# Kernel optimization log

Measured on AMD Instinct MI355X. Metric: run time of the kernel, lower is better.

The kernel has to match this reference:

```python
import jax, jax.numpy as jnp
import numpy as np

D_MODEL = 1024
NUM_HEADS = 16
D_K = D_MODEL // NUM_HEADS
CLAMP = 1e9
EPS = 1e-12


def setup_inputs() -> dict:
    key = jax.random.key(0)
    ks = jax.random.split(key, 11)
    B, S, D = 4, 2048, D_MODEL
    std = 1.0 / np.sqrt(D)
    inp = {
        'Q': jax.random.normal(ks[0], (B, S, D), jnp.float32),
        'K': jax.random.normal(ks[1], (B, S, D), jnp.float32),
        'V': jax.random.normal(ks[2], (B, S, D), jnp.float32),
        'Wq': jax.random.normal(ks[3], (D, D), jnp.float32) * std,
        'bq': jnp.zeros((D,), jnp.float32),
        'Wk': jax.random.normal(ks[4], (D, D), jnp.float32) * std,
        'bk': jnp.zeros((D,), jnp.float32),
        'Wv': jax.random.normal(ks[5], (D, D), jnp.float32) * std,
        'bv': jnp.zeros((D,), jnp.float32),
        'Wo': jax.random.normal(ks[6], (D, D), jnp.float32) * std,
        'bo': jnp.zeros((D,), jnp.float32),
    }
    return inp


def _split_heads(x):
    b, s, _ = x.shape
    return x.reshape(b, s, NUM_HEADS, D_K).transpose(0, 2, 1, 3)  # [b,h,s,dk]


def reference(Q, K, V, Wq, bq, Wk, bk, Wv, bv, Wo, bo):
    Qh = _split_heads(Q @ Wq.T + bq)
    Kh = _split_heads(K @ Wk.T + bk)
    Vh = _split_heads(V @ Wv.T + bv)
    scale = jnp.sqrt(jnp.asarray(D_K, Qh.dtype))
    scores = jnp.einsum('bhqd,bhkd->bhqk', Qh, Kh) / scale
    scores = scores - jnp.max(scores, axis=-1, keepdims=True)
    scores = jnp.clip(scores, -CLAMP, CLAMP)
    attn = jax.nn.softmax(scores, axis=-1)
    attn = jnp.clip(attn, EPS, None)
    attn = attn / jnp.sum(attn, axis=-1, keepdims=True)
    ctx = jnp.einsum('bhqk,bhkd->bhqd', attn, Vh)
    b, h, s, dk = ctx.shape
    ctx = ctx.transpose(0, 2, 1, 3).reshape(b, s, D_MODEL)
    return ctx @ Wo.T + bo
```

## Files before the change

kernel.cpp:

```cpp
#include <hip/hip_runtime.h>
#include <hip/hip_bf16.h>


typedef float  f32x4  __attribute__((ext_vector_type(4)));
typedef __bf16 bf16x8 __attribute__((ext_vector_type(8)));
typedef short  s16x8  __attribute__((ext_vector_type(8)));
typedef int    i32x4  __attribute__((ext_vector_type(4)));

#define MFMA16(a,b,c) __builtin_amdgcn_mfma_f32_16x16x32_bf16((a),(b),(c),0,0,0)

__device__ __forceinline__ unsigned short f2bf(float f) {
    union { float f; unsigned u; } v; v.f = f;
    unsigned r = v.u + 0x7fffu + ((v.u >> 16) & 1u);
    return (unsigned short)(r >> 16);
}

__device__ __forceinline__ s16x8 cvt8(const float* __restrict__ p) {
    f32x4 x = *(const f32x4*)p;
    f32x4 y = *(const f32x4*)(p + 4);
    s16x8 r;
    r[0] = (short)f2bf(x[0]); r[1] = (short)f2bf(x[1]);
    r[2] = (short)f2bf(x[2]); r[3] = (short)f2bf(x[3]);
    r[4] = (short)f2bf(y[0]); r[5] = (short)f2bf(y[1]);
    r[6] = (short)f2bf(y[2]); r[7] = (short)f2bf(y[3]);
    return r;
}

__device__ __forceinline__ void gl_lds16(const void* g, void* l) {
    __builtin_amdgcn_global_load_lds(
        (const __attribute__((address_space(1))) unsigned int*)g,
        (__attribute__((address_space(3))) unsigned int*)l, 16, 0, 0);
}

__device__ __forceinline__ int cvtpk_bf16(float lo, float hi) {
    int r;
    asm("v_cvt_pk_bf16_f32 %0, %1, %2" : "=v"(r) : "v"(lo), "v"(hi));
    return r;
}
__device__ __forceinline__ void plswap32(int& a, int& b) {
    asm("v_permlane32_swap_b32 %0, %1" : "+v"(a), "+v"(b));
}
__device__ __forceinline__ void plswap16(int& a, int& b) {
    asm("v_permlane16_swap_b32 %0, %1" : "+v"(a), "+v"(b));
}

__global__ __launch_bounds__(256) void cvt_kernel(
    const float* __restrict__ src, unsigned short* __restrict__ dst, int n8)
{
    int i = blockIdx.x * 256 + threadIdx.x;
    if (i < n8) *(s16x8*)(dst + (size_t)i * 8) = cvt8(src + (size_t)i * 8);
}

template <int MODE>
__global__ __launch_bounds__(256) void gemm_bf16(
    const unsigned short* __restrict__ A,
    const unsigned short* __restrict__ W,
    const float* __restrict__ bias,
    void* __restrict__ Cv)
{
    constexpr int K = 1024;
    __shared__ unsigned short Ash[128 * 32];
    __shared__ unsigned short Bsh[128 * 32];

    const int t    = threadIdx.x;
    const int w    = t >> 6;
    const int lane = t & 63;
    const int wm   = w >> 1, wn = w & 1;
    const int lr   = lane & 15, quad = lane >> 4;

    const int m0 = blockIdx.y * 128;
    const int n0 = blockIdx.x * 128;

    const int srow = t >> 2;
    const int skp  = (t & 3) * 8;

    const unsigned short* Ap0 = A + (size_t)(m0 + srow) * K + skp;
    const unsigned short* Ap1 = Ap0 + (size_t)64 * K;
    const unsigned short* Wp0 = W + (size_t)(n0 + srow) * K + skp;
    const unsigned short* Wp1 = Wp0 + (size_t)64 * K;
    unsigned short* lA0 = &Ash[w * 512];
    unsigned short* lA1 = &Ash[2048 + w * 512];
    unsigned short* lB0 = &Bsh[w * 512];
    unsigned short* lB1 = &Bsh[2048 + w * 512];

    f32x4 acc[4][4] = {};

    for (int k0 = 0; k0 < K; k0 += 32) {
        __syncthreads();
        gl_lds16(Ap0 + k0, lA0);
        gl_lds16(Ap1 + k0, lA1);
        gl_lds16(Wp0 + k0, lB0);
        gl_lds16(Wp1 + k0, lB1);
        __syncthreads();

        bf16x8 af[4], bw[4];
#pragma unroll
        for (int i = 0; i < 4; i++)
            af[i] = *(const bf16x8*)&Ash[(wm * 64 + i * 16 + lr) * 32 + quad * 8];
#pragma unroll
        for (int j = 0; j < 4; j++)
            bw[j] = *(const bf16x8*)&Bsh[(wn * 64 + j * 16 + lr) * 32 + quad * 8];

#pragma unroll
        for (int i = 0; i < 4; i++)
#pragma unroll
            for (int j = 0; j < 4; j++)
                acc[i][j] = MFMA16(af[i], bw[j], acc[i][j]);
    }

#pragma unroll
    for (int i = 0; i < 4; i++) {
#pragma unroll
        for (int j = 0; j < 4; j++) {
            const int n = n0 + wn * 64 + j * 16 + lr;
#pragma unroll
            for (int r = 0; r < 4; r++) {
                const int m = m0 + wm * 64 + i * 16 + quad * 4 + r;
                float val = acc[i][j][r] + ((MODE == 2) ? bias[m] : bias[n]);
                if (MODE == 0) {
                    const int b = m >> 11, s = m & 2047, h = n >> 6, d = n & 63;
                    ((unsigned short*)Cv)[(((size_t)(b * 16 + h) * 2048 + s) << 6) + d] = f2bf(val);
                } else if (MODE == 1) {
                    ((float*)Cv)[(size_t)m * 1024 + n] = val;
                } else {
                    const int h = m >> 6, d = m & 63, b = n >> 11, s = n & 2047;
                    ((unsigned short*)Cv)[((size_t)(b * 16 + h) * 64 + d) * 2048 + s] = f2bf(val);
                }
            }
        }
    }
}

__global__ __launch_bounds__(256) void attn_kernel(
    const unsigned short* __restrict__ Qh,
    const unsigned short* __restrict__ Kh,
    const unsigned short* __restrict__ Vt,
    unsigned short* __restrict__ ctx)
{
    constexpr int KS = 72;
    __shared__ unsigned short Ksh[64 * KS];
    __shared__ unsigned short Vts[64 * KS];

    const int t    = threadIdx.x;
    const int w    = t >> 6;
    const int lane = t & 63;
    const int lr   = lane & 15, quad = lane >> 4;

    const int bh = blockIdx.y, qblk = blockIdx.x;
    const size_t base = (size_t)bh * 2048 * 64;
    const unsigned short* Qp = Qh + base;
    const unsigned short* Kg = Kh + base + (size_t)lane * 64 + w * 16;
    const unsigned short* Vg = Vt + base + (size_t)lane * 2048 + w * 16;

    const int q0 = qblk * 64 + w * 16;
    bf16x8 aq0 = *(const bf16x8*)(Qp + (size_t)(q0 + lr) * 64 + quad * 8);
    bf16x8 aq1 = *(const bf16x8*)(Qp + (size_t)(q0 + lr) * 64 + 32 + quad * 8);

    f32x4 Of[4] = {};
    float lsum = 0.f;

    s16x8 kv0 = *(const s16x8*)(Kg);
    s16x8 kv1 = *(const s16x8*)(Kg + 8);
    s16x8 vv0 = *(const s16x8*)(Vg);
    s16x8 vv1 = *(const s16x8*)(Vg + 8);

    for (int kb = 0; kb < 2048; kb += 64) {
        __syncthreads();
        *(s16x8*)&Ksh[lane * KS + w * 16]     = kv0;
        *(s16x8*)&Ksh[lane * KS + w * 16 + 8] = kv1;
        *(s16x8*)&Vts[lane * KS + w * 16]     = vv0;
        *(s16x8*)&Vts[lane * KS + w * 16 + 8] = vv1;

        const int kn = (kb + 64) & 2047;
        kv0 = *(const s16x8*)(Kg + (size_t)kn * 64);
        kv1 = *(const s16x8*)(Kg + (size_t)kn * 64 + 8);
        vv0 = *(const s16x8*)(Vg + kn);
        vv1 = *(const s16x8*)(Vg + kn + 8);

        __syncthreads();

        f32x4 pe[4];
#pragma unroll
        for (int nt = 0; nt < 4; nt++) {
            const unsigned short* kr = &Ksh[(16 * nt + lr) * KS + quad * 8];
            f32x4 c = {};
            c = MFMA16(*(const bf16x8*)kr, aq0, c);
            c = MFMA16(*(const bf16x8*)(kr + 32), aq1, c);
            f32x4 p;
#pragma unroll
            for (int r = 0; r < 4; r++) p[r] = __expf(c[r] * 0.125f);
            lsum += (p[0] + p[1]) + (p[2] + p[3]);
            pe[nt] = p;
        }

        int a0 = cvtpk_bf16(pe[0][0], pe[0][1]);
        int a1 = cvtpk_bf16(pe[0][2], pe[0][3]);
        int b0 = cvtpk_bf16(pe[1][0], pe[1][1]);
        int b1 = cvtpk_bf16(pe[1][2], pe[1][3]);
        plswap32(a0, b0); plswap32(a1, b1);
        plswap16(a0, b0); plswap16(a1, b1);
        i32x4 f0; f0[0] = a0; f0[1] = a1; f0[2] = b0; f0[3] = b1;

        int c0 = cvtpk_bf16(pe[2][0], pe[2][1]);
        int c1 = cvtpk_bf16(pe[2][2], pe[2][3]);
        int d0 = cvtpk_bf16(pe[3][0], pe[3][1]);
        int d1 = cvtpk_bf16(pe[3][2], pe[3][3]);
        plswap32(c0, d0); plswap32(c1, d1);
        plswap16(c0, d0); plswap16(c1, d1);
        i32x4 f1; f1[0] = c0; f1[1] = c1; f1[2] = d0; f1[3] = d1;

        bf16x8 pf0 = __builtin_bit_cast(bf16x8, f0);
        bf16x8 pf1 = __builtin_bit_cast(bf16x8, f1);

#pragma unroll
        for (int dt = 0; dt < 4; dt++) {
            const unsigned short* vr = &Vts[(dt * 16 + lr) * KS + quad * 8];
            Of[dt] = MFMA16(pf0, *(const bf16x8*)vr, Of[dt]);
            Of[dt] = MFMA16(pf1, *(const bf16x8*)(vr + 32), Of[dt]);
        }
    }

    lsum += __shfl_xor(lsum, 16);
    lsum += __shfl_xor(lsum, 32);

    const int b = bh >> 4, h = bh & 15;
#pragma unroll
    for (int r = 0; r < 4; r++) {
        const float inv = 1.0f / __shfl(lsum, quad * 4 + r, 64);
        const int q = q0 + quad * 4 + r;
        unsigned short* cp = ctx + ((size_t)b * 2048 + q) * 1024 + h * 64;
#pragma unroll
        for (int dt = 0; dt < 4; dt++)
            cp[dt * 16 + lr] = f2bf(Of[dt][r] * inv);
    }
}

extern "C" void kernel_launch(void* const* d_in, const int* in_sizes, int n_in,
                              void* d_out, int out_size, void* d_ws, size_t ws_size,
                              hipStream_t stream) {
    const float* Q  = (const float*)d_in[0];
    const float* K  = (const float*)d_in[1];
    const float* V  = (const float*)d_in[2];
    const float* Wq = (const float*)d_in[3];
    const float* bq = (const float*)d_in[4];
    const float* Wk = (const float*)d_in[5];
    const float* bk = (const float*)d_in[6];
    const float* Wv = (const float*)d_in[7];
    const float* bv = (const float*)d_in[8];
    const float* Wo = (const float*)d_in[9];
    const float* bo = (const float*)d_in[10];

    const size_t EB = (size_t)8192 * 1024;
    const size_t EW = (size_t)1024 * 1024;
    unsigned short* Xb  = (unsigned short*)d_ws;
    unsigned short* Wqb = Xb  + EB;
    unsigned short* Wkb = Wqb + EW;
    unsigned short* Wvb = Wkb + EW;
    unsigned short* Wob = Wvb + EW;
    unsigned short* Qh  = Wob + EW;
    unsigned short* Kh  = Qh  + EB;
    unsigned short* Vtw = Kh  + EB;
    unsigned short* Ctx = Xb;

    const int n8b = (int)(EB / 8);
    const int n8w = (int)(EW / 8);

    cvt_kernel<<<n8w / 256, 256, 0, stream>>>(Wq, Wqb, n8w);
    cvt_kernel<<<n8w / 256, 256, 0, stream>>>(Wk, Wkb, n8w);
    cvt_kernel<<<n8w / 256, 256, 0, stream>>>(Wv, Wvb, n8w);
    cvt_kernel<<<n8w / 256, 256, 0, stream>>>(Wo, Wob, n8w);

    dim3 tb(256), gP(8, 64), gT(64, 8);

    cvt_kernel<<<n8b / 256, 256, 0, stream>>>(Q, Xb, n8b);
    gemm_bf16<0><<<gP, tb, 0, stream>>>(Xb, Wqb, bq, Qh);

    cvt_kernel<<<n8b / 256, 256, 0, stream>>>(K, Xb, n8b);
    gemm_bf16<0><<<gP, tb, 0, stream>>>(Xb, Wkb, bk, Kh);

    cvt_kernel<<<n8b / 256, 256, 0, stream>>>(V, Xb, n8b);
    gemm_bf16<2><<<gT, tb, 0, stream>>>(Wvb, Xb, bv, Vtw);

    attn_kernel<<<dim3(32, 64), tb, 0, stream>>>(Qh, Kh, Vtw, Ctx);

    gemm_bf16<1><<<gP, tb, 0, stream>>>(Ctx, Wob, bo, (float*)d_out);
}
```

Baseline: 422.4 us.

## Process 32 query rows per wave in attention and fold softmax scale into Q

Each attention wave now handles two 16-row query tiles instead of one, so every K and V fragment read from shared memory feeds twice as many MFMAs. The grid is halved to match. The 1/sqrt(dk)·log2(e) factor is folded into the Q projection epilogue, so the inner loop can use a raw v_exp_f32 (exp2) without a per-element multiply. The cost is more accumulator registers per wave and fewer blocks, which may lower occupancy. Q is also rounded to bf16 after scaling, which slightly changes numerics.

```diff
diff --git a/kernel.cpp b/kernel.cpp
--- a/kernel.cpp
+++ b/kernel.cpp
@@ -32,6 +32,12 @@
         (__attribute__((address_space(3))) unsigned int*)l, 16, 0, 0);
 }
 
+__device__ __forceinline__ float exp2_fast(float x) {
+    float r;
+    asm("v_exp_f32 %0, %1" : "=v"(r) : "v"(x));
+    return r;
+}
+
 __device__ __forceinline__ int cvtpk_bf16(float lo, float hi) {
     int r;
     asm("v_cvt_pk_bf16_f32 %0, %1, %2" : "=v"(r) : "v"(lo), "v"(hi));
@@ -42,6 +48,25 @@
 }
 __device__ __forceinline__ void plswap16(int& a, int& b) {
     asm("v_permlane16_swap_b32 %0, %1" : "+v"(a), "+v"(b));
+}
+
+__device__ __forceinline__ void pack_pf(const f32x4 pe[4], bf16x8& pf0, bf16x8& pf1) {
+    int a0 = cvtpk_bf16(pe[0][0], pe[0][1]);
+    int a1 = cvtpk_bf16(pe[0][2], pe[0][3]);
+    int b0 = cvtpk_bf16(pe[1][0], pe[1][1]);
+    int b1 = cvtpk_bf16(pe[1][2], pe[1][3]);
+    plswap32(a0, b0); plswap32(a1, b1);
+    plswap16(a0, b0); plswap16(a1, b1);
+    i32x4 f0; f0[0] = a0; f0[1] = a1; f0[2] = b0; f0[3] = b1;
+    int c0 = cvtpk_bf16(pe[2][0], pe[2][1]);
+    int c1 = cvtpk_bf16(pe[2][2], pe[2][3]);
+    int d0 = cvtpk_bf16(pe[3][0], pe[3][1]);
+    int d1 = cvtpk_bf16(pe[3][2], pe[3][3]);
+    plswap32(c0, d0); plswap32(c1, d1);
+    plswap16(c0, d0); plswap16(c1, d1);
+    i32x4 f1; f1[0] = c0; f1[1] = c1; f1[2] = d0; f1[3] = d1;
+    pf0 = __builtin_bit_cast(bf16x8, f0);
+    pf1 = __builtin_bit_cast(bf16x8, f1);
 }
 
 __global__ __launch_bounds__(256) void cvt_kernel(
@@ -56,7 +81,7 @@
     const unsigned short* __restrict__ A,
     const unsigned short* __restrict__ W,
     const float* __restrict__ bias,
-    void* __restrict__ Cv)
+    void* __restrict__ Cv, float scale)
 {
     constexpr int K = 1024;
     __shared__ unsigned short Ash[128 * 32];
@@ -116,7 +141,7 @@
 #pragma unroll
             for (int r = 0; r < 4; r++) {
                 const int m = m0 + wm * 64 + i * 16 + quad * 4 + r;
-                float val = acc[i][j][r] + ((MODE == 2) ? bias[m] : bias[n]);
+                float val = (acc[i][j][r] + ((MODE == 2) ? bias[m] : bias[n])) * scale;
                 if (MODE == 0) {
                     const int b = m >> 11, s = m & 2047, h = n >> 6, d = n & 63;
                     ((unsigned short*)Cv)[(((size_t)(b * 16 + h) * 2048 + s) << 6) + d] = f2bf(val);
@@ -152,12 +177,16 @@
     const unsigned short* Kg = Kh + base + (size_t)lane * 64 + w * 16;
     const unsigned short* Vg = Vt + base + (size_t)lane * 2048 + w * 16;
 
-    const int q0 = qblk * 64 + w * 16;
-    bf16x8 aq0 = *(const bf16x8*)(Qp + (size_t)(q0 + lr) * 64 + quad * 8);
-    bf16x8 aq1 = *(const bf16x8*)(Qp + (size_t)(q0 + lr) * 64 + 32 + quad * 8);
-
-    f32x4 Of[4] = {};
-    float lsum = 0.f;
+    const int q0 = qblk * 128 + w * 32;
+    const unsigned short* qr0 = Qp + (size_t)(q0 + lr) * 64;
+    const unsigned short* qr1 = Qp + (size_t)(q0 + 16 + lr) * 64;
+    bf16x8 aq0 = *(const bf16x8*)(qr0 + quad * 8);
+    bf16x8 aq1 = *(const bf16x8*)(qr0 + 32 + quad * 8);
+    bf16x8 aq2 = *(const bf16x8*)(qr1 + quad * 8);
+    bf16x8 aq3 = *(const bf16x8*)(qr1 + 32 + quad * 8);
+
+    f32x4 Of0[4] = {}, Of1[4] = {};
+    float ls0 = 0.f, ls1 = 0.f;
 
     s16x8 kv0 = *(const s16x8*)(Kg);
     s16x8 kv1 = *(const s16x8*)(Kg + 8);
@@ -179,59 +208,62 @@
 
         __syncthreads();
 
-        f32x4 pe[4];
+        f32x4 pe0[4], pe1[4];
 #pragma unroll
         for (int nt = 0; nt < 4; nt++) {
             const unsigned short* kr = &Ksh[(16 * nt + lr) * KS + quad * 8];
-            f32x4 c = {};
-            c = MFMA16(*(const bf16x8*)kr, aq0, c);
-            c = MFMA16(*(const bf16x8*)(kr + 32), aq1, c);
-            f32x4 p;
-#pragma unroll
-            for (int r = 0; r < 4; r++) p[r] = __expf(c[r] * 0.125f);
-            lsum += (p[0] + p[1]) + (p[2] + p[3]);
-            pe[nt] = p;
+            bf16x8 k0 = *(const bf16x8*)kr;
+            bf16x8 k1 = *(const bf16x8*)(kr + 32);
+            f32x4 c0 = {}, c1 = {};
+            c0 = MFMA16(k0, aq0, c0); c0 = MFMA16(k1, aq1, c0);
+            c1 = MFMA16(k0, aq2, c1); c1 = MFMA16(k1, aq3, c1);
+            f32x4 p0, p1;
+#pragma unroll
+            for (int r = 0; r < 4; r++) p0[r] = exp2_fast(c0[r]);
+#pragma unroll
+            for (int r = 0; r < 4; r++) p1[r] = exp2_fast(c1[r]);
+            ls0 += (p0[0] + p0[1]) + (p0[2] + p0[3]);
+            ls1 += (p1[0] + p1[1]) + (p1[2] + p1[3]);
+            pe0[nt] = p0; pe1[nt] = p1;
         }
 
-        int a0 = cvtpk_bf16(pe[0][0], pe[0][1]);
-        int a1 = cvtpk_bf16(pe[0][2], pe[0][3]);
-        int b0 = cvtpk_bf16(pe[1][0], pe[1][1]);
-        int b1 = cvtpk_bf16(pe[1][2], pe[1][3]);
-        plswap32(a0, b0); plswap32(a1, b1);
-        plswap16(a0, b0); plswap16(a1, b1);
-        i32x4 f0; f0[0] = a0; f0[1] = a1; f0[2] = b0; f0[3] = b1;
-
-        int c0 = cvtpk_bf16(pe[2][0], pe[2][1]);
-        int c1 = cvtpk_bf16(pe[2][2], pe[2][3]);
-        int d0 = cvtpk_bf16(pe[3][0], pe[3][1]);
-        int d1 = cvtpk_bf16(pe[3][2], pe[3][3]);
-        plswap32(c0, d0); plswap32(c1, d1);
-        plswap16(c0, d0); plswap16(c1, d1);
-        i32x4 f1; f1[0] = c0; f1[1] = c1; f1[2] = d0; f1[3] = d1;
-
-        bf16x8 pf0 = __builtin_bit_cast(bf16x8, f0);
-        bf16x8 pf1 = __builtin_bit_cast(bf16x8, f1);
+        bf16x8 pf00, pf01, pf10, pf11;
+        pack_pf(pe0, pf00, pf01);
+        pack_pf(pe1, pf10, pf11);
 
 #pragma unroll
         for (int dt = 0; dt < 4; dt++) {
             const unsigned short* vr = &Vts[(dt * 16 + lr) * KS + quad * 8];
-            Of[dt] = MFMA16(pf0, *(const bf16x8*)vr, Of[dt]);
-            Of[dt] = MFMA16(pf1, *(const bf16x8*)(vr + 32), Of[dt]);
+            bf16x8 v0 = *(const bf16x8*)vr;
+            bf16x8 v1 = *(const bf16x8*)(vr + 32);
+            Of0[dt] = MFMA16(pf00, v0, Of0[dt]);
+            Of0[dt] = MFMA16(pf01, v1, Of0[dt]);
+            Of1[dt] = MFMA16(pf10, v0, Of1[dt]);
+            Of1[dt] = MFMA16(pf11, v1, Of1[dt]);
         }
     }
 
-    lsum += __shfl_xor(lsum, 16);
-    lsum += __shfl_xor(lsum, 32);
+    ls0 += __shfl_xor(ls0, 16);
+    ls0 += __shfl_xor(ls0, 32);
+    ls1 += __shfl_xor(ls1, 16);
+    ls1 += __shfl_xor(ls1, 32);
 
     const int b = bh >> 4, h = bh & 15;
 #pragma unroll
     for (int r = 0; r < 4; r++) {
-        const float inv = 1.0f / __shfl(lsum, quad * 4 + r, 64);
-        const int q = q0 + quad * 4 + r;
-        unsigned short* cp = ctx + ((size_t)b * 2048 + q) * 1024 + h * 64;
+        const float inv0 = 1.0f / __shfl(ls0, quad * 4 + r, 64);
+        const int qa = q0 + quad * 4 + r;
+        unsigned short* cp0 = ctx + ((size_t)b * 2048 + qa) * 1024 + h * 64;
 #pragma unroll
         for (int dt = 0; dt < 4; dt++)
-            cp[dt * 16 + lr] = f2bf(Of[dt][r] * inv);
+            cp0[dt * 16 + lr] = f2bf(Of0[dt][r] * inv0);
+
+        const float inv1 = 1.0f / __shfl(ls1, quad * 4 + r, 64);
+        const int qb = q0 + 16 + quad * 4 + r;
+        unsigned short* cp1 = ctx + ((size_t)b * 2048 + qb) * 1024 + h * 64;
+#pragma unroll
+        for (int dt = 0; dt < 4; dt++)
+            cp1[dt * 16 + lr] = f2bf(Of1[dt][r] * inv1);
     }
 }
 
@@ -265,6 +297,8 @@
     const int n8b = (int)(EB / 8);
     const int n8w = (int)(EW / 8);
 
+    const float QSCALE = 0.125f * 1.44269504088896340736f;
+
     cvt_kernel<<<n8w / 256, 256, 0, stream>>>(Wq, Wqb, n8w);
     cvt_kernel<<<n8w / 256, 256, 0, stream>>>(Wk, Wkb, n8w);
     cvt_kernel<<<n8w / 256, 256, 0, stream>>>(Wv, Wvb, n8w);
@@ -273,15 +307,15 @@
     dim3 tb(256), gP(8, 64), gT(64, 8);
 
     cvt_kernel<<<n8b / 256, 256, 0, stream>>>(Q, Xb, n8b);
-    gemm_bf16<0><<<gP, tb, 0, stream>>>(Xb, Wqb, bq, Qh);
+    gemm_bf16<0><<<gP, tb, 0, stream>>>(Xb, Wqb, bq, Qh, QSCALE);
 
     cvt_kernel<<<n8b / 256, 256, 0, stream>>>(K, Xb, n8b);
-    gemm_bf16<0><<<gP, tb, 0, stream>>>(Xb, Wkb, bk, Kh);
+    gemm_bf16<0><<<gP, tb, 0, stream>>>(Xb, Wkb, bk, Kh, 1.0f);
 
     cvt_kernel<<<n8b / 256, 256, 0, stream>>>(V, Xb, n8b);
-    gemm_bf16<2><<<gT, tb, 0, stream>>>(Wvb, Xb, bv, Vtw);
-
-    attn_kernel<<<dim3(32, 64), tb, 0, stream>>>(Qh, Kh, Vtw, Ctx);
-
-    gemm_bf16<1><<<gP, tb, 0, stream>>>(Ctx, Wob, bo, (float*)d_out);
-}
+    gemm_bf16<2><<<gT, tb, 0, stream>>>(Wvb, Xb, bv, Vtw, 1.0f);
+
+    attn_kernel<<<dim3(16, 64), tb, 0, stream>>>(Qh, Kh, Vtw, Ctx);
+
+    gemm_bf16<1><<<gP, tb, 0, stream>>>(Ctx, Wob, bo, (float*)d_out, 1.0f);
+}
```

Result: faster. 373.0 us (-11.7%).
